# Kernel tuning notes

Hardware: AMD Instinct MI355X
Metric: run time of the kernel (lower is better)

Reference implementation:

```python
import jax, jax.numpy as jnp
import numpy as np

EMB_DIM = 1024
N_HEAD = 16
HEAD_DIM = EMB_DIM // N_HEAD


def setup_inputs() -> dict:
    key = jax.random.key(0)
    k1, k2, k3, k4, k5 = jax.random.split(key, 5)
    x = jax.random.normal(k1, (4, 2048, EMB_DIM), dtype=jnp.float32)
    s = 1.0 / np.sqrt(EMB_DIM)
    W_qkv = jax.random.uniform(k2, (3 * EMB_DIM, EMB_DIM), minval=-s, maxval=s, dtype=jnp.float32)
    b_qkv = jax.random.uniform(k3, (3 * EMB_DIM,), minval=-s, maxval=s, dtype=jnp.float32)
    W_proj = jax.random.uniform(k4, (EMB_DIM, EMB_DIM), minval=-s, maxval=s, dtype=jnp.float32)
    b_proj = jax.random.uniform(k5, (EMB_DIM,), minval=-s, maxval=s, dtype=jnp.float32)
    return {"x": x, "W_qkv": W_qkv, "b_qkv": b_qkv, "W_proj": W_proj, "b_proj": b_proj}


def reference(x, W_qkv, b_qkv, W_proj, b_proj):
    B, S, E = x.shape
    H, D = N_HEAD, HEAD_DIM
    qkv = x @ W_qkv.T + b_qkv  # [B,S,3E]
    q, k, v = jnp.split(qkv, 3, axis=-1)
    # [B,S,E] -> [B,H,S,D]
    q = q.reshape(B, S, H, D).transpose(0, 2, 1, 3)
    k = k.reshape(B, S, H, D).transpose(0, 2, 1, 3)
    v = v.reshape(B, S, H, D).transpose(0, 2, 1, 3)
    scale = 1.0 / jnp.sqrt(jnp.asarray(D, dtype=x.dtype))
    scores = jnp.einsum('bhqd,bhkd->bhqk', q, k) * scale
    causal = jnp.tril(jnp.ones((S, S), dtype=bool))
    scores = jnp.where(causal, scores, jnp.asarray(-jnp.inf, dtype=scores.dtype))
    attn = jax.nn.softmax(scores, axis=-1)
    y = jnp.einsum('bhqk,bhkd->bhqd', attn, v)  # [B,H,S,D]
    y = y.transpose(0, 2, 1, 3).reshape(B, S, E)
    return y @ W_proj.T + b_proj
```

## Files before the change

kernel.cpp:

```cpp
#include <hip/hip_runtime.h>
#include <hip/hip_bf16.h>

typedef __attribute__((ext_vector_type(4))) float f32x4;
typedef __attribute__((ext_vector_type(8))) __bf16 bf16x8;
typedef __attribute__((ext_vector_type(4))) unsigned int u32x4;

#define EMB 1024
#define NHEAD 16
#define HDIM 64
#define SEQ 2048
#define BATCH 4
#define NTOK 8192

__device__ __forceinline__ unsigned short f2bf(float f) {
    unsigned int u = __builtin_bit_cast(unsigned int, f);
    u = (u + 0x7fffu + ((u >> 16) & 1u)) >> 16;
    return (unsigned short)u;
}

__device__ __forceinline__ unsigned int cvt2_bf16(float lo, float hi) {
    unsigned short a = __builtin_bit_cast(unsigned short, (__bf16)lo);
    unsigned short b = __builtin_bit_cast(unsigned short, (__bf16)hi);
    return (unsigned int)a | ((unsigned int)b << 16);
}

__device__ __forceinline__ unsigned long long pack_bf4(const f32x4 v) {
    unsigned long long lo = cvt2_bf16(v[0], v[1]);
    unsigned long long hi = cvt2_bf16(v[2], v[3]);
    return lo | (hi << 32);
}

__device__ __forceinline__ void async_copy16(const ushort* g, ushort* l) {
    __builtin_amdgcn_global_load_lds(
        (const __attribute__((address_space(1))) void*)g,
        (__attribute__((address_space(3))) void*)l,
        16, 0, 0);
}

__global__ void cvt_f32_bf16(const float4* __restrict__ in, ushort* __restrict__ out, int n4) {
    int i = blockIdx.x * 256 + threadIdx.x;
    if (i < n4) {
        float4 v = in[i];
        ushort4 o;
        o.x = f2bf(v.x); o.y = f2bf(v.y); o.z = f2bf(v.z); o.w = f2bf(v.w);
        ((ushort4*)out)[i] = o;
    }
}

#define GEMM_STAGE64(Asrc, Bsrc, m0, n0, kt)                                      \
    {                                                                             \
        _Pragma("unroll")                                                         \
        for (int j = 0; j < 2; ++j) {                                             \
            int row = wave * 32 + j * 16 + (lane >> 2);                           \
            int kc  = (lane & 3) ^ ((row >> 1) & 3);                              \
            const ushort* asrc = Asrc + (size_t)(m0 + row) * EMB + kt + kc * 8;   \
            const ushort* bsrc = Bsrc + (size_t)(n0 + row) * EMB + kt + kc * 8;   \
            async_copy16(asrc,      As0 + (wave * 32 + j * 16) * 32);             \
            async_copy16(asrc + 32, As1 + (wave * 32 + j * 16) * 32);             \
            async_copy16(bsrc,      Bs0 + (wave * 32 + j * 16) * 32);             \
            async_copy16(bsrc + 32, Bs1 + (wave * 32 + j * 16) * 32);             \
        }                                                                         \
    }

#define GEMM_BODY64(Asrc, Bsrc, m0, n0)                                           \
    f32x4 acc[4][4] = {};                                                         \
    for (int kt = 0; kt < EMB; kt += 64) {                                        \
        GEMM_STAGE64(Asrc, Bsrc, m0, n0, kt)                                      \
        __syncthreads();                                                          \
        _Pragma("unroll")                                                         \
        for (int hf = 0; hf < 2; ++hf) {                                          \
            const ushort* Ah = hf ? As1 : As0;                                    \
            const ushort* Bh = hf ? Bs1 : Bs0;                                    \
            bf16x8 a[4], b[4];                                                    \
            _Pragma("unroll")                                                     \
            for (int i = 0; i < 4; ++i) {                                         \
                int r = wm + i * 16 + col;                                        \
                a[i] = *(const bf16x8*)&Ah[r * 32 + (quad ^ ((r >> 1) & 3)) * 8]; \
                int c = wn + i * 16 + col;                                        \
                b[i] = *(const bf16x8*)&Bh[c * 32 + (quad ^ ((c >> 1) & 3)) * 8]; \
            }                                                                     \
            _Pragma("unroll")                                                     \
            for (int i = 0; i < 4; ++i)                                           \
                _Pragma("unroll")                                                 \
                for (int j = 0; j < 4; ++j)                                       \
                    acc[i][j] = __builtin_amdgcn_mfma_f32_16x16x32_bf16(          \
                        a[i], b[j], acc[i][j], 0, 0, 0);                          \
        }                                                                         \
        __syncthreads();                                                          \
    }

__global__ __launch_bounds__(256) void gemm_qk(
    const ushort* __restrict__ A,
    const ushort* __restrict__ W,
    const float*  __restrict__ bias,
    ushort* __restrict__ Qb, ushort* __restrict__ Kb)
{
    __shared__ ushort As0[128 * 32];
    __shared__ ushort As1[128 * 32];
    __shared__ ushort Bs0[128 * 32];
    __shared__ ushort Bs1[128 * 32];
    const int tid  = threadIdx.x;
    const int lane = tid & 63;
    const int wave = tid >> 6;
    const int col  = lane & 15;
    const int quad = lane >> 4;
    const int m0 = blockIdx.x * 128;
    const int n0 = blockIdx.y * 128;
    const int wm = (wave >> 1) * 64;
    const int wn = (wave & 1) * 64;

    GEMM_BODY64(A, W, m0, n0)

    #pragma unroll
    for (int i = 0; i < 4; ++i)
        #pragma unroll
        for (int j = 0; j < 4; ++j)
            #pragma unroll
            for (int r = 0; r < 4; ++r) {
                int m = m0 + wm + i * 16 + quad * 4 + r;
                int n = n0 + wn + j * 16 + col;
                float v = acc[i][j][r] + bias[n];
                unsigned short bv = f2bf(v);
                int e = n & 1023;
                int h = e >> 6, d = e & 63;
                int b = m >> 11, s = m & 2047;
                size_t bh = (size_t)(b * NHEAD + h);
                if (n < 1024) Qb[(bh * SEQ + s) * HDIM + d] = bv;
                else          Kb[(bh * SEQ + s) * HDIM + d] = bv;
            }
}

__global__ __launch_bounds__(256) void gemm_vt(
    const ushort* __restrict__ Wv,
    const ushort* __restrict__ X,
    const float*  __restrict__ bias,
    ushort* __restrict__ Vtx)
{
    __shared__ ushort As0[128 * 32];
    __shared__ ushort As1[128 * 32];
    __shared__ ushort Bs0[128 * 32];
    __shared__ ushort Bs1[128 * 32];
    const int tid  = threadIdx.x;
    const int lane = tid & 63;
    const int wave = tid >> 6;
    const int col  = lane & 15;
    const int quad = lane >> 4;
    const int m0 = blockIdx.x * 128;
    const int n0 = blockIdx.y * 128;
    const int wm = (wave >> 1) * 64;
    const int wn = (wave & 1) * 64;

    GEMM_BODY64(Wv, X, m0, n0)

    #pragma unroll
    for (int i = 0; i < 4; ++i)
        #pragma unroll
        for (int j = 0; j < 4; ++j)
            #pragma unroll
            for (int r = 0; r < 4; ++r) {
                int m = m0 + wm + i * 16 + quad * 4 + r;
                int n = n0 + wn + j * 16 + col;
                Vtx[(size_t)m * NTOK + n] = f2bf(acc[i][j][r] + bias[m]);
            }
}

__global__ __launch_bounds__(256) void gemm_proj(
    const ushort* __restrict__ A,
    const ushort* __restrict__ W,
    const float*  __restrict__ bias,
    float* __restrict__ out)
{
    __shared__ ushort As0[128 * 32];
    __shared__ ushort As1[128 * 32];
    __shared__ ushort Bs0[128 * 32];
    __shared__ ushort Bs1[128 * 32];
    const int tid  = threadIdx.x;
    const int lane = tid & 63;
    const int wave = tid >> 6;
    const int col  = lane & 15;
    const int quad = lane >> 4;
    const int m0 = blockIdx.x * 128;
    const int n0 = blockIdx.y * 128;
    const int wm = (wave >> 1) * 64;
    const int wn = (wave & 1) * 64;

    GEMM_BODY64(A, W, m0, n0)

    #pragma unroll
    for (int i = 0; i < 4; ++i)
        #pragma unroll
        for (int j = 0; j < 4; ++j)
            #pragma unroll
            for (int r = 0; r < 4; ++r) {
                int m = m0 + wm + i * 16 + quad * 4 + r;
                int n = n0 + wn + j * 16 + col;
                out[(size_t)m * EMB + n] = acc[i][j][r] + bias[n];
            }
}

__device__ __forceinline__ void attn_qtile(
    int qt, int b, int h, int lane, int wave,
    const ushort* __restrict__ Qh, const ushort* __restrict__ Kh,
    const ushort* __restrict__ Vh, ushort* __restrict__ Yb,
    ushort* __restrict__ Ks0, ushort* __restrict__ Ks1, ushort* __restrict__ Vs,
    ushort* __restrict__ Ps)
{
    const int col  = lane & 15;
    const int quad = lane >> 4;
    const int q0   = qt * 128 + wave * 32;
    const float SC = 0.125f * 1.44269504f;

    bf16x8 qf[2][2];
    #pragma unroll
    for (int g = 0; g < 2; ++g) {
        const ushort* qp = Qh + (size_t)(q0 + g * 16 + col) * HDIM;
        qf[g][0] = *(const bf16x8*)(qp + quad * 8);
        qf[g][1] = *(const bf16x8*)(qp + 32 + quad * 8);
    }

    ushort* Pw = Ps + wave * 2048;

    f32x4 o[2][4] = {};
    float lrun[2] = {0.f, 0.f};

    const int nk = qt + 1;
    for (int kt = 0; kt < nk; ++kt) {
        const int k0 = kt * 128;
        const bool last = (kt == nk - 1);

        {
            int srow = wave * 16 + (lane >> 2);
            #pragma unroll
            for (int rr = 0; rr < 2; ++rr) {
                int r = rr * 64 + srow;
                int kc = (lane & 3) ^ ((r >> 1) & 3);
                const ushort* src = Kh + (size_t)(k0 + r) * HDIM + kc * 8;
                async_copy16(src,      Ks0 + (rr * 64 + wave * 16) * 32);
                async_copy16(src + 32, Ks1 + (rr * 64 + wave * 16) * 32);
            }
            int kc = (lane & 3) ^ ((srow >> 1) & 3);
            const ushort* vsrc = Vh + (size_t)srow * NTOK + k0 + kc * 8;
            #pragma unroll
            for (int kq = 0; kq < 4; ++kq)
                async_copy16(vsrc + kq * 32, Vs + kq * 2048 + (wave * 16) * 32);
        }
        __syncthreads();

        f32x4 st[2][8];
        #pragma unroll
        for (int j = 0; j < 8; ++j) {
            int r = j * 16 + col;
            int q_ = (quad ^ ((r >> 1) & 3)) * 8;
            bf16x8 kf0 = *(const bf16x8*)&Ks0[r * 32 + q_];
            bf16x8 kf1 = *(const bf16x8*)&Ks1[r * 32 + q_];
            #pragma unroll
            for (int g = 0; g < 2; ++g) {
                f32x4 z = {0.f, 0.f, 0.f, 0.f};
                f32x4 t = __builtin_amdgcn_mfma_f32_16x16x32_bf16(kf0, qf[g][0], z, 0, 0, 0);
                st[g][j] = __builtin_amdgcn_mfma_f32_16x16x32_bf16(kf1, qf[g][1], t, 0, 0, 0);
            }
        }

        if (last) {
            #pragma unroll
            for (int g = 0; g < 2; ++g) {
                int rowg = q0 + g * 16 + col;
                #pragma unroll
                for (int j = 0; j < 8; ++j)
                    #pragma unroll
                    for (int r = 0; r < 4; ++r) {
                        float pv = __builtin_amdgcn_exp2f(st[g][j][r] * SC);
                        int c = k0 + j * 16 + quad * 4 + r;
                        pv = (c <= rowg) ? pv : 0.f;
                        st[g][j][r] = pv;
                        lrun[g] += pv;
                    }
            }
        } else {
            #pragma unroll
            for (int g = 0; g < 2; ++g)
                #pragma unroll
                for (int j = 0; j < 8; ++j)
                    #pragma unroll
                    for (int r = 0; r < 4; ++r) {
                        float pv = __builtin_amdgcn_exp2f(st[g][j][r] * SC);
                        st[g][j][r] = pv;
                        lrun[g] += pv;
                    }
        }

        bf16x8 pf[2][4];
        #pragma unroll
        for (int g = 0; g < 2; ++g) {
            #pragma unroll
            for (int j = 0; j < 8; ++j) {
                int blk = 2 * j + (quad >> 1);
                *(unsigned long long*)&Pw[col * 128 + ((blk ^ col) & 15) * 8 + (quad & 1) * 4]
                    = pack_bf4(st[g][j]);
            }
            #pragma unroll
            for (int kq = 0; kq < 4; ++kq) {
                int blk = 4 * kq + quad;
                pf[g][kq] = *(const bf16x8*)&Pw[col * 128 + ((blk ^ col) & 15) * 8];
            }
        }

        #pragma unroll
        for (int dt = 0; dt < 4; ++dt) {
            int r = dt * 16 + col;
            int q_ = (quad ^ ((r >> 1) & 3)) * 8;
            #pragma unroll
            for (int kq = 0; kq < 4; ++kq) {
                bf16x8 vf = *(const bf16x8*)&Vs[kq * 2048 + r * 32 + q_];
                o[0][dt] = __builtin_amdgcn_mfma_f32_16x16x32_bf16(vf, pf[0][kq], o[0][dt], 0, 0, 0);
                o[1][dt] = __builtin_amdgcn_mfma_f32_16x16x32_bf16(vf, pf[1][kq], o[1][dt], 0, 0, 0);
            }
        }
        __syncthreads();
    }

    #pragma unroll
    for (int g = 0; g < 2; ++g) {
        float l = lrun[g];
        l += __shfl_xor(l, 16, 64);
        l += __shfl_xor(l, 32, 64);
        float inv = 1.f / l;
        int rowg = q0 + g * 16 + col;
        size_t rbase = ((size_t)(b * SEQ + rowg)) * EMB + h * HDIM + quad * 4;
        #pragma unroll
        for (int dt = 0; dt < 4; ++dt) {
            ushort4 s4;
            s4.x = f2bf(o[g][dt][0] * inv);
            s4.y = f2bf(o[g][dt][1] * inv);
            s4.z = f2bf(o[g][dt][2] * inv);
            s4.w = f2bf(o[g][dt][3] * inv);
            *(ushort4*)(Yb + rbase + dt * 16) = s4;
        }
    }
}

__global__ __launch_bounds__(256, 2) void attn(
    const ushort* __restrict__ Qb, const ushort* __restrict__ Kb,
    const ushort* __restrict__ Vtx, ushort* __restrict__ Yb)
{
    __shared__ ushort Ks0[128 * 32];
    __shared__ ushort Ks1[128 * 32];
    __shared__ ushort Vs[4 * 64 * 32];
    __shared__ __align__(16) ushort Ps[4 * 2048];
    const int lane = threadIdx.x & 63;
    const int wave = threadIdx.x >> 6;
    const int bh   = blockIdx.x & 63;
    const int pr   = blockIdx.x >> 6;

    const int b = bh >> 4, h = bh & 15;
    const ushort* Qh = Qb + (size_t)bh * SEQ * HDIM;
    const ushort* Kh = Kb + (size_t)bh * SEQ * HDIM;
    const ushort* Vh = Vtx + (size_t)(h * HDIM) * NTOK + b * SEQ;

    attn_qtile(15 - pr, b, h, lane, wave, Qh, Kh, Vh, Yb, Ks0, Ks1, Vs, Ps);
    __syncthreads();
    attn_qtile(pr,      b, h, lane, wave, Qh, Kh, Vh, Yb, Ks0, Ks1, Vs, Ps);
}

extern "C" void kernel_launch(void* const* d_in, const int* in_sizes, int n_in,
                              void* d_out, int out_size, void* d_ws, size_t ws_size,
                              hipStream_t stream) {
    const float* x      = (const float*)d_in[0];
    const float* W_qkv  = (const float*)d_in[1];
    const float* b_qkv  = (const float*)d_in[2];
    const float* W_proj = (const float*)d_in[3];
    const float* b_proj = (const float*)d_in[4];
    float* out = (float*)d_out;

    ushort* ws     = (ushort*)d_ws;
    ushort* Xb     = ws;
    ushort* Yb     = ws;
    ushort* Wqkvb  = ws + 8388608;
    ushort* Wprojb = ws + 11534336;
    ushort* Qb     = ws + 12582912;
    ushort* Kb     = ws + 20971520;
    ushort* Vtx    = ws + 29360128;

    cvt_f32_bf16<<<8192, 256, 0, stream>>>((const float4*)x,      Xb,     2097152);
    cvt_f32_bf16<<<3072, 256, 0, stream>>>((const float4*)W_qkv,  Wqkvb,  786432);
    cvt_f32_bf16<<<1024, 256, 0, stream>>>((const float4*)W_proj, Wprojb, 262144);

    gemm_qk<<<dim3(64, 16), 256, 0, stream>>>(Xb, Wqkvb, b_qkv, Qb, Kb);
    gemm_vt<<<dim3(8, 64), 256, 0, stream>>>(Wqkvb + (size_t)2048 * EMB, Xb,
                                             b_qkv + 2048, Vtx);
    attn<<<512, 256, 0, stream>>>(Qb, Kb, Vtx, Yb);
    gemm_proj<<<dim3(64, 8), 256, 0, stream>>>(Yb, Wprojb, b_proj, out);
}
```

Before: 245.8 us.

## Switch attention to 32x32x16 MFMA and keep P in registers via permlane swap

Rewrites the attention inner loop to use 32x32x16 bf16 MFMA tiles, so each wave's 32 query rows map onto a single 32-wide tile. The P matrix is converted to bf16 and rearranged across lane halves with v_permlane32_swap, then fed directly as the MFMA operand. This removes the per-wave LDS round-trip for P and the Ps shared buffer, which cuts LDS traffic and shared memory use. The cost is a more complex register layout in which each lane holds 16-element accumulators, which may raise register pressure.

```diff
diff --git a/kernel.cpp b/kernel.cpp
--- a/kernel.cpp
+++ b/kernel.cpp
@@ -2,6 +2,7 @@
 #include <hip/hip_bf16.h>
 
 typedef __attribute__((ext_vector_type(4))) float f32x4;
+typedef __attribute__((ext_vector_type(16))) float f32x16;
 typedef __attribute__((ext_vector_type(8))) __bf16 bf16x8;
 typedef __attribute__((ext_vector_type(4))) unsigned int u32x4;
 
@@ -24,10 +25,8 @@
     return (unsigned int)a | ((unsigned int)b << 16);
 }
 
-__device__ __forceinline__ unsigned long long pack_bf4(const f32x4 v) {
-    unsigned long long lo = cvt2_bf16(v[0], v[1]);
-    unsigned long long hi = cvt2_bf16(v[2], v[3]);
-    return lo | (hi << 32);
+__device__ __forceinline__ void permlane32_swap(unsigned int &x, unsigned int &y) {
+    asm volatile("v_permlane32_swap_b32 %0, %1" : "+v"(x), "+v"(y));
 }
 
 __device__ __forceinline__ void async_copy16(const ushort* g, ushort* l) {
@@ -202,26 +201,21 @@
     int qt, int b, int h, int lane, int wave,
     const ushort* __restrict__ Qh, const ushort* __restrict__ Kh,
     const ushort* __restrict__ Vh, ushort* __restrict__ Yb,
-    ushort* __restrict__ Ks0, ushort* __restrict__ Ks1, ushort* __restrict__ Vs,
-    ushort* __restrict__ Ps)
-{
-    const int col  = lane & 15;
-    const int quad = lane >> 4;
-    const int q0   = qt * 128 + wave * 32;
+    ushort* __restrict__ Ks0, ushort* __restrict__ Ks1, ushort* __restrict__ Vs)
+{
+    const int ql = lane & 31;
+    const int hi = lane >> 5;
+    const int q0 = qt * 128 + wave * 32;
+    const int qrow = q0 + ql;
     const float SC = 0.125f * 1.44269504f;
 
-    bf16x8 qf[2][2];
-    #pragma unroll
-    for (int g = 0; g < 2; ++g) {
-        const ushort* qp = Qh + (size_t)(q0 + g * 16 + col) * HDIM;
-        qf[g][0] = *(const bf16x8*)(qp + quad * 8);
-        qf[g][1] = *(const bf16x8*)(qp + 32 + quad * 8);
-    }
-
-    ushort* Pw = Ps + wave * 2048;
-
-    f32x4 o[2][4] = {};
-    float lrun[2] = {0.f, 0.f};
+    bf16x8 qb[4];
+    #pragma unroll
+    for (int c = 0; c < 4; ++c)
+        qb[c] = *(const bf16x8*)(Qh + (size_t)qrow * HDIM + c * 16 + hi * 8);
+
+    f32x16 o2[2] = {};
+    float lrun = 0.f;
 
     const int nk = qt + 1;
     for (int kt = 0; kt < nk; ++kt) {
@@ -246,97 +240,86 @@
         }
         __syncthreads();
 
-        f32x4 st[2][8];
-        #pragma unroll
-        for (int j = 0; j < 8; ++j) {
-            int r = j * 16 + col;
-            int q_ = (quad ^ ((r >> 1) & 3)) * 8;
-            bf16x8 kf0 = *(const bf16x8*)&Ks0[r * 32 + q_];
-            bf16x8 kf1 = *(const bf16x8*)&Ks1[r * 32 + q_];
-            #pragma unroll
-            for (int g = 0; g < 2; ++g) {
-                f32x4 z = {0.f, 0.f, 0.f, 0.f};
-                f32x4 t = __builtin_amdgcn_mfma_f32_16x16x32_bf16(kf0, qf[g][0], z, 0, 0, 0);
-                st[g][j] = __builtin_amdgcn_mfma_f32_16x16x32_bf16(kf1, qf[g][1], t, 0, 0, 0);
-            }
+        f32x16 st[4];
+        #pragma unroll
+        for (int t = 0; t < 4; ++t) {
+            f32x16 acc = {};
+            #pragma unroll
+            for (int c = 0; c < 4; ++c) {
+                int row = t * 32 + ql;
+                int swz = ((c & 1) * 2 + hi) ^ ((row >> 1) & 3);
+                const ushort* Kbase = (c < 2) ? Ks0 : Ks1;
+                bf16x8 kf = *(const bf16x8*)&Kbase[row * 32 + swz * 8];
+                acc = __builtin_amdgcn_mfma_f32_32x32x16_bf16(kf, qb[c], acc, 0, 0, 0);
+            }
+            st[t] = acc;
         }
 
         if (last) {
             #pragma unroll
-            for (int g = 0; g < 2; ++g) {
-                int rowg = q0 + g * 16 + col;
+            for (int t = 0; t < 4; ++t)
                 #pragma unroll
-                for (int j = 0; j < 8; ++j)
-                    #pragma unroll
-                    for (int r = 0; r < 4; ++r) {
-                        float pv = __builtin_amdgcn_exp2f(st[g][j][r] * SC);
-                        int c = k0 + j * 16 + quad * 4 + r;
-                        pv = (c <= rowg) ? pv : 0.f;
-                        st[g][j][r] = pv;
-                        lrun[g] += pv;
-                    }
-            }
+                for (int r = 0; r < 16; ++r) {
+                    float pv = __builtin_amdgcn_exp2f(st[t][r] * SC);
+                    int key = k0 + t * 32 + (r & 3) + 8 * (r >> 2) + 4 * hi;
+                    pv = (key <= qrow) ? pv : 0.f;
+                    st[t][r] = pv;
+                    lrun += pv;
+                }
         } else {
             #pragma unroll
-            for (int g = 0; g < 2; ++g)
+            for (int t = 0; t < 4; ++t)
                 #pragma unroll
-                for (int j = 0; j < 8; ++j)
-                    #pragma unroll
-                    for (int r = 0; r < 4; ++r) {
-                        float pv = __builtin_amdgcn_exp2f(st[g][j][r] * SC);
-                        st[g][j][r] = pv;
-                        lrun[g] += pv;
-                    }
-        }
-
-        bf16x8 pf[2][4];
-        #pragma unroll
-        for (int g = 0; g < 2; ++g) {
-            #pragma unroll
-            for (int j = 0; j < 8; ++j) {
-                int blk = 2 * j + (quad >> 1);
-                *(unsigned long long*)&Pw[col * 128 + ((blk ^ col) & 15) * 8 + (quad & 1) * 4]
-                    = pack_bf4(st[g][j]);
-            }
-            #pragma unroll
-            for (int kq = 0; kq < 4; ++kq) {
-                int blk = 4 * kq + quad;
-                pf[g][kq] = *(const bf16x8*)&Pw[col * 128 + ((blk ^ col) & 15) * 8];
-            }
-        }
-
-        #pragma unroll
-        for (int dt = 0; dt < 4; ++dt) {
-            int r = dt * 16 + col;
-            int q_ = (quad ^ ((r >> 1) & 3)) * 8;
-            #pragma unroll
-            for (int kq = 0; kq < 4; ++kq) {
-                bf16x8 vf = *(const bf16x8*)&Vs[kq * 2048 + r * 32 + q_];
-                o[0][dt] = __builtin_amdgcn_mfma_f32_16x16x32_bf16(vf, pf[0][kq], o[0][dt], 0, 0, 0);
-                o[1][dt] = __builtin_amdgcn_mfma_f32_16x16x32_bf16(vf, pf[1][kq], o[1][dt], 0, 0, 0);
+                for (int r = 0; r < 16; ++r) {
+                    float pv = __builtin_amdgcn_exp2f(st[t][r] * SC);
+                    st[t][r] = pv;
+                    lrun += pv;
+                }
+        }
+
+        #pragma unroll
+        for (int t = 0; t < 4; ++t) {
+            unsigned int Ap[4], Bp[4];
+            #pragma unroll
+            for (int m = 0; m < 4; ++m) {
+                Ap[m] = cvt2_bf16(st[t][4 * m],     st[t][4 * m + 1]);
+                Bp[m] = cvt2_bf16(st[t][4 * m + 2], st[t][4 * m + 3]);
+            }
+            #pragma unroll
+            for (int kc = 0; kc < 2; ++kc) {
+                unsigned int xa = Ap[2 * kc], ya = Ap[2 * kc + 1];
+                unsigned int xb = Bp[2 * kc], yb = Bp[2 * kc + 1];
+                permlane32_swap(xa, ya);
+                permlane32_swap(xb, yb);
+                u32x4 pw; pw[0] = xa; pw[1] = xb; pw[2] = ya; pw[3] = yb;
+                bf16x8 pf = __builtin_bit_cast(bf16x8, pw);
+                #pragma unroll
+                for (int dt = 0; dt < 2; ++dt) {
+                    int row = dt * 32 + ql;
+                    int swz = (kc * 2 + hi) ^ ((row >> 1) & 3);
+                    bf16x8 vf = *(const bf16x8*)&Vs[t * 2048 + row * 32 + swz * 8];
+                    o2[dt] = __builtin_amdgcn_mfma_f32_32x32x16_bf16(vf, pf, o2[dt], 0, 0, 0);
+                }
             }
         }
         __syncthreads();
     }
 
-    #pragma unroll
-    for (int g = 0; g < 2; ++g) {
-        float l = lrun[g];
-        l += __shfl_xor(l, 16, 64);
-        l += __shfl_xor(l, 32, 64);
-        float inv = 1.f / l;
-        int rowg = q0 + g * 16 + col;
-        size_t rbase = ((size_t)(b * SEQ + rowg)) * EMB + h * HDIM + quad * 4;
-        #pragma unroll
-        for (int dt = 0; dt < 4; ++dt) {
+    lrun += __shfl_xor(lrun, 32, 64);
+    float inv = 1.f / lrun;
+    size_t rbase = ((size_t)(b * SEQ + qrow)) * EMB + h * HDIM;
+    #pragma unroll
+    for (int dt = 0; dt < 2; ++dt)
+        #pragma unroll
+        for (int m = 0; m < 4; ++m) {
+            int d = dt * 32 + 8 * m + 4 * hi;
             ushort4 s4;
-            s4.x = f2bf(o[g][dt][0] * inv);
-            s4.y = f2bf(o[g][dt][1] * inv);
-            s4.z = f2bf(o[g][dt][2] * inv);
-            s4.w = f2bf(o[g][dt][3] * inv);
-            *(ushort4*)(Yb + rbase + dt * 16) = s4;
-        }
-    }
+            s4.x = f2bf(o2[dt][4 * m]     * inv);
+            s4.y = f2bf(o2[dt][4 * m + 1] * inv);
+            s4.z = f2bf(o2[dt][4 * m + 2] * inv);
+            s4.w = f2bf(o2[dt][4 * m + 3] * inv);
+            *(ushort4*)(Yb + rbase + d) = s4;
+        }
 }
 
 __global__ __launch_bounds__(256, 2) void attn(
@@ -346,7 +329,6 @@
     __shared__ ushort Ks0[128 * 32];
     __shared__ ushort Ks1[128 * 32];
     __shared__ ushort Vs[4 * 64 * 32];
-    __shared__ __align__(16) ushort Ps[4 * 2048];
     const int lane = threadIdx.x & 63;
     const int wave = threadIdx.x >> 6;
     const int bh   = blockIdx.x & 63;
@@ -357,9 +339,9 @@
     const ushort* Kh = Kb + (size_t)bh * SEQ * HDIM;
     const ushort* Vh = Vtx + (size_t)(h * HDIM) * NTOK + b * SEQ;
 
-    attn_qtile(15 - pr, b, h, lane, wave, Qh, Kh, Vh, Yb, Ks0, Ks1, Vs, Ps);
+    attn_qtile(15 - pr, b, h, lane, wave, Qh, Kh, Vh, Yb, Ks0, Ks1, Vs);
     __syncthreads();
-    attn_qtile(pr,      b, h, lane, wave, Qh, Kh, Vh, Yb, Ks0, Ks1, Vs, Ps);
+    attn_qtile(pr,      b, h, lane, wave, Qh, Kh, Vh, Yb, Ks0, Ks1, Vs);
 }
 
 extern "C" void kernel_launch(void* const* d_in, const int* in_sizes, int n_in,
```

Result: no change. 244.7 us (-0.5%).
